# Optimization experiments

Hardware: AMD Instinct MI355X
Metric: run time of the kernel (lower is better)

Reference implementation:

```python
import jax, jax.numpy as jnp
import numpy as np

N = 4096
NFEAT = 512
NHID = 64
NHEADS = 8
NCLASS = 41
ALPHA = 0.2          # LeakyReLU negative slope
NEG = -9e15          # mask fill value from the torch code
EDGE_P = 0.004       # ~16 avg degree


def _xavier_uniform(key, shape, gain=1.414):
    fan_in, fan_out = shape[-2], shape[-1]
    limit = gain * np.sqrt(6.0 / (fan_in + fan_out))
    return jax.random.uniform(key, shape, jnp.float32, -limit, limit)


def setup_inputs() -> dict:
    key = jax.random.key(0)
    ks = jax.random.split(key, 6)
    x = jax.random.normal(ks[0], (N, NFEAT), jnp.float32)
    # sparse random graph, densified (module calls adj.to_dense()); add self-loops
    adj = (jax.random.uniform(ks[1], (N, N)) < EDGE_P).astype(jnp.float32)
    adj = jnp.maximum(adj, jnp.eye(N, dtype=jnp.float32))
    # 8 attention heads (nfeat -> nhid), stacked
    W_heads = _xavier_uniform(ks[2], (NHEADS, NFEAT, NHID))
    a_heads = _xavier_uniform(ks[3], (NHEADS, 2 * NHID, 1))
    # output attention layer (nhid*nheads -> nclass)
    W_out = _xavier_uniform(ks[4], (NHEADS * NHID, NCLASS))
    a_out = _xavier_uniform(ks[5], (2 * NCLASS, 1))
    return {"x": x, "adj": adj, "W_heads": W_heads, "a_heads": a_heads,
            "W_out": W_out, "a_out": a_out}


def _leaky_relu(e):
    return jnp.where(e > 0, e, ALPHA * e)


def reference(x, adj, W_heads, a_heads, W_out, a_out):
    # inference mode: all dropout layers are identity (training=False)
    mask = adj > 0                                   # [N, N]
    # ---- multi-head GAT layer (concat=True, ELU inside layer) ----
    Wh = jnp.einsum('nf,hfd->hnd', x, W_heads)       # [H, N, D]
    a1 = a_heads[:, :NHID, 0]                        # [H, D]
    a2 = a_heads[:, NHID:, 0]                        # [H, D]
    s1 = jnp.einsum('hnd,hd->hn', Wh, a1)            # [H, N]
    s2 = jnp.einsum('hnd,hd->hn', Wh, a2)            # [H, N]
    e = _leaky_relu(s1[:, :, None] + s2[:, None, :])  # [H, N, N]
    att = jax.nn.softmax(jnp.where(mask[None], e, NEG), axis=-1)
    h = jax.nn.elu(jnp.einsum('hnm,hmd->hnd', att, Wh))   # [H, N, D]
    h = jnp.transpose(h, (1, 0, 2)).reshape(N, NHEADS * NHID)  # concat heads
    # ---- output GAT layer (concat=False) + ELU (with_relu=True) ----
    Wh2 = h @ W_out                                  # [N, C]
    e2 = _leaky_relu(Wh2 @ a_out[:NCLASS] + (Wh2 @ a_out[NCLASS:]).T)  # [N, N]
    att2 = jax.nn.softmax(jnp.where(mask, e2, NEG), axis=-1)
    out = jax.nn.elu(att2 @ Wh2)                     # [N, C]
    # mode='t', multi_label falsy -> log_softmax
    return jax.nn.log_softmax(out, axis=1)
```

## Files before the change

kernel.cpp:

```cpp
#include <hip/hip_runtime.h>
#include <hip/hip_bf16.h>
#include <math.h>


#define N 4096
#define NFEAT 512
#define NHID 64
#define NHEADS 8
#define NCLASS 41
#define NCPAD 48
#define ALPHA 0.2f
#define ELLW 64

using short8  = __attribute__((ext_vector_type(8))) short;
using floatx4 = __attribute__((ext_vector_type(4))) float;

__device__ __forceinline__ float wred_max(float v) {
#pragma unroll
  for (int o = 32; o; o >>= 1) v = fmaxf(v, __shfl_xor(v, o, 64));
  return v;
}
__device__ __forceinline__ float wred_sum(float v) {
#pragma unroll
  for (int o = 32; o; o >>= 1) v += __shfl_xor(v, o, 64);
  return v;
}

__device__ __forceinline__ void split_bf16(float v, short& hi, short& lo) {
  __hip_bfloat16 hb = __float2bfloat16(v);
  float hf = __bfloat162float(hb);
  __hip_bfloat16 lb = __float2bfloat16(v - hf);
  hi = *reinterpret_cast<short*>(&hb);
  lo = *reinterpret_cast<short*>(&lb);
}

__global__ __launch_bounds__(256) void setup(const float* __restrict__ x,
                                             const float* __restrict__ W,
                                             const float* __restrict__ W_out,
                                             const float* __restrict__ adj,
                                             short* __restrict__ Xhi,
                                             short* __restrict__ Xlo,
                                             short* __restrict__ Wthi,
                                             short* __restrict__ Wtlo,
                                             short* __restrict__ WOhi,
                                             short* __restrict__ WOlo,
                                             int* __restrict__ cols,
                                             int* __restrict__ cnts) {
  if (blockIdx.x < 4096) {
    __shared__ int c;
    const int row = blockIdx.x;
    if (threadIdx.x == 0) c = 0;
    __syncthreads();
    const float4* arow = (const float4*)(adj + (size_t)row * N);
    for (int j4 = threadIdx.x; j4 < N / 4; j4 += 256) {
      float4 v = arow[j4];
      if (v.x > 0.f) { int p = atomicAdd(&c, 1); if (p < ELLW) cols[row * ELLW + p] = j4 * 4 + 0; }
      if (v.y > 0.f) { int p = atomicAdd(&c, 1); if (p < ELLW) cols[row * ELLW + p] = j4 * 4 + 1; }
      if (v.z > 0.f) { int p = atomicAdd(&c, 1); if (p < ELLW) cols[row * ELLW + p] = j4 * 4 + 2; }
      if (v.w > 0.f) { int p = atomicAdd(&c, 1); if (p < ELLW) cols[row * ELLW + p] = j4 * 4 + 3; }
    }
    __syncthreads();
    if (threadIdx.x == 0) cnts[row] = min(c, ELLW);
  } else if (blockIdx.x < 6144) {
    const int t = (blockIdx.x - 4096) * 256 + threadIdx.x;
    const float4 v = ((const float4*)x)[t];
    short h0, l0, h1, l1, h2, l2, h3, l3;
    split_bf16(v.x, h0, l0);
    split_bf16(v.y, h1, l1);
    split_bf16(v.z, h2, l2);
    split_bf16(v.w, h3, l3);
    ((short4*)Xhi)[t] = make_short4(h0, h1, h2, h3);
    ((short4*)Xlo)[t] = make_short4(l0, l1, l2, l3);
  } else if (blockIdx.x < 6208) {
    __shared__ float tile[64][65];
    const int idx = blockIdx.x - 6144;
    const int h = idx >> 3, k0 = (idx & 7) * 64;
    const int t = threadIdx.x;
#pragma unroll
    for (int i = 0; i < 4; i++) {
      const int g = t + 256 * i;
      const int r = g >> 4, c4 = g & 15;
      const float4 v = *(const float4*)&W[(size_t)h * 32768 + (size_t)(k0 + r) * 64 + c4 * 4];
      tile[r][c4 * 4 + 0] = v.x;
      tile[r][c4 * 4 + 1] = v.y;
      tile[r][c4 * 4 + 2] = v.z;
      tile[r][c4 * 4 + 3] = v.w;
    }
    __syncthreads();
#pragma unroll
    for (int i = 0; i < 2; i++) {
      const int g = t + 256 * i;
      const int d = g >> 3, kg = (g & 7) * 8;
      short8 hv, lv;
#pragma unroll
      for (int j = 0; j < 8; j++) {
        short hh, ll;
        split_bf16(tile[kg + j][d], hh, ll);
        hv[j] = hh;
        lv[j] = ll;
      }
      const size_t dst = (size_t)h * 32768 + (size_t)d * 512 + k0 + kg;
      *(short8*)&Wthi[dst] = hv;
      *(short8*)&Wtlo[dst] = lv;
    }
  } else {
    const int t = (blockIdx.x - 6208) * 256 + threadIdx.x;
    const int c = t >> 9, k = t & 511;
    float v = (c < NCLASS) ? W_out[(size_t)k * NCLASS + c] : 0.f;
    short hi, lo;
    split_bf16(v, hi, lo);
    WOhi[c * 512 + k] = hi;
    WOlo[c * 512 + k] = lo;
  }
}

__global__ __launch_bounds__(256) void wh_gemm_mfma(
    const short* __restrict__ Xhi, const short* __restrict__ Xlo,
    const short* __restrict__ Wthi, const short* __restrict__ Wtlo,
    const float* __restrict__ a_heads,
    float* __restrict__ Wh, float* __restrict__ s1, float* __restrict__ s2) {
  const int id = blockIdx.x;
  const int h = (id >> 3) & 7;
  const int tile = (id & 7) + ((id >> 6) << 3);
  const int n0 = tile * 64;
  const int w = threadIdx.x >> 6, L = threadIdx.x & 63;
  const int q = L >> 4, r15 = L & 15;

  floatx4 acc[4];
#pragma unroll
  for (int f = 0; f < 4; f++) acc[f] = (floatx4){0.f, 0.f, 0.f, 0.f};

  const short* Ah = Xhi + (size_t)(n0 + w * 16 + r15) * NFEAT;
  const short* Al = Xlo + (size_t)(n0 + w * 16 + r15) * NFEAT;
  const short* Bh = Wthi + (size_t)h * 32768 + (size_t)r15 * 512;
  const short* Bl = Wtlo + (size_t)h * 32768 + (size_t)r15 * 512;

#pragma unroll 2
  for (int ks = 0; ks < 16; ks++) {
    const int ko = ks * 32 + q * 8;
    const short8 ahi = *(const short8*)&Ah[ko];
    const short8 alo = *(const short8*)&Al[ko];
#pragma unroll
    for (int f = 0; f < 4; f++) {
      const short8 bhi = *(const short8*)&Bh[f * 16 * 512 + ko];
      const short8 blo = *(const short8*)&Bl[f * 16 * 512 + ko];
      acc[f] = __builtin_amdgcn_mfma_f32_16x16x32_bf16(ahi, bhi, acc[f], 0, 0, 0);
      acc[f] = __builtin_amdgcn_mfma_f32_16x16x32_bf16(ahi, blo, acc[f], 0, 0, 0);
      acc[f] = __builtin_amdgcn_mfma_f32_16x16x32_bf16(alo, bhi, acc[f], 0, 0, 0);
    }
  }

  const int c16 = r15;
  float a1v[4], a2v[4];
#pragma unroll
  for (int f = 0; f < 4; f++) {
    a1v[f] = a_heads[h * 128 + f * 16 + c16];
    a2v[f] = a_heads[h * 128 + 64 + f * 16 + c16];
  }
  float p1[4] = {0.f, 0.f, 0.f, 0.f}, p2[4] = {0.f, 0.f, 0.f, 0.f};
#pragma unroll
  for (int f = 0; f < 4; f++)
#pragma unroll
    for (int r = 0; r < 4; r++) {
      const float vv = acc[f][r];
      const int row = n0 + w * 16 + q * 4 + r;
      Wh[((size_t)(h << 12) + row) * NHID + f * 16 + c16] = vv;
      p1[r] += vv * a1v[f];
      p2[r] += vv * a2v[f];
    }
#pragma unroll
  for (int r = 0; r < 4; r++)
#pragma unroll
    for (int o = 1; o < 16; o <<= 1) {
      p1[r] += __shfl_xor(p1[r], o, 64);
      p2[r] += __shfl_xor(p2[r], o, 64);
    }
  if (c16 == 0) {
    const int row = n0 + w * 16 + q * 4;
#pragma unroll
    for (int r = 0; r < 4; r++) {
      s1[(h << 12) + row + r] = p1[r];
      s2[(h << 12) + row + r] = p2[r];
    }
  }
}

__global__ __launch_bounds__(256) void att1_kernel(
    const float* __restrict__ Wh, const float* __restrict__ s1,
    const float* __restrict__ s2, const int* __restrict__ cols,
    const int* __restrict__ cnts, short* __restrict__ Hhi,
    short* __restrict__ Hlo) {
  __shared__ float pj[4][64];
  __shared__ int jj[4][64];
  const int w = threadIdx.x >> 6, lane = threadIdx.x & 63;
  const int pair = blockIdx.x * 4 + w;
  const int h = pair >> 12, i = pair & (N - 1);
  const int cnt = cnts[i];
  const float s1i = s1[(h << 12) + i];
  const float* s2h = s2 + (h << 12);
  float e0 = -1e30f;
  int j0 = 0;
  if (lane < cnt) {
    j0 = cols[i * ELLW + lane];
    float t = s1i + s2h[j0];
    e0 = t > 0.f ? t : ALPHA * t;
  }
  const float m = wred_max(e0);
  float p = (lane < cnt) ? expf(e0 - m) : 0.f;
  const float S = wred_sum(p);
  p *= 1.f / S;
  pj[w][lane] = p;
  jj[w][lane] = (lane < cnt) ? j0 : 0;
  __syncthreads();
  const int grp = lane >> 3, c8 = lane & 7;
  const float* Whh = Wh + (((size_t)h << 12)) * NHID;
  float4 a0 = make_float4(0.f, 0.f, 0.f, 0.f);
  float4 a1 = make_float4(0.f, 0.f, 0.f, 0.f);
  for (int t0 = 0; t0 < cnt; t0 += 8) {
    const float pt = pj[w][t0 + grp];
    const int jt = jj[w][t0 + grp];
    const float4 v0 = *(const float4*)&Whh[(size_t)jt * NHID + c8 * 8];
    const float4 v1 = *(const float4*)&Whh[(size_t)jt * NHID + c8 * 8 + 4];
    a0.x += pt * v0.x; a0.y += pt * v0.y; a0.z += pt * v0.z; a0.w += pt * v0.w;
    a1.x += pt * v1.x; a1.y += pt * v1.y; a1.z += pt * v1.z; a1.w += pt * v1.w;
  }
#pragma unroll
  for (int off = 8; off <= 32; off <<= 1) {
    a0.x += __shfl_xor(a0.x, off, 64);
    a0.y += __shfl_xor(a0.y, off, 64);
    a0.z += __shfl_xor(a0.z, off, 64);
    a0.w += __shfl_xor(a0.w, off, 64);
    a1.x += __shfl_xor(a1.x, off, 64);
    a1.y += __shfl_xor(a1.y, off, 64);
    a1.z += __shfl_xor(a1.z, off, 64);
    a1.w += __shfl_xor(a1.w, off, 64);
  }
  if (grp == 0) {
    float o[8] = {a0.x, a0.y, a0.z, a0.w, a1.x, a1.y, a1.z, a1.w};
    short8 hv, lv;
#pragma unroll
    for (int j = 0; j < 8; j++) {
      const float e = o[j] > 0.f ? o[j] : expf(o[j]) - 1.f;
      short hh, ll;
      split_bf16(e, hh, ll);
      hv[j] = hh;
      lv[j] = ll;
    }
    const size_t base = (size_t)i * 512 + h * 64 + c8 * 8;
    *(short8*)&Hhi[base] = hv;
    *(short8*)&Hlo[base] = lv;
  }
}

__global__ __launch_bounds__(256) void gemm2_mfma(
    const short* __restrict__ Hhi, const short* __restrict__ Hlo,
    const short* __restrict__ WOhi, const short* __restrict__ WOlo,
    const float* __restrict__ a_out,
    float* __restrict__ Wh2, float* __restrict__ s1b, float* __restrict__ s2b) {
  __shared__ float red[3][64][12];
  const int n0 = blockIdx.x * 16;
  const int tid = threadIdx.x;
  const int w = tid >> 6, L = tid & 63;
  const int r15 = L & 15;

  floatx4 acc[3];
#pragma unroll
  for (int f = 0; f < 3; f++) acc[f] = (floatx4){0.f, 0.f, 0.f, 0.f};

#pragma unroll
  for (int ks = 0; ks < 4; ks++) {
    const int koff = w * 128 + ks * 32 + (L >> 4) * 8;
    const short8 ahi = *(const short8*)&Hhi[(size_t)(n0 + r15) * 512 + koff];
    const short8 alo = *(const short8*)&Hlo[(size_t)(n0 + r15) * 512 + koff];
#pragma unroll
    for (int f = 0; f < 3; f++) {
      const short8 bhi = *(const short8*)&WOhi[(size_t)(f * 16 + r15) * 512 + koff];
      const short8 blo = *(const short8*)&WOlo[(size_t)(f * 16 + r15) * 512 + koff];
      acc[f] = __builtin_amdgcn_mfma_f32_16x16x32_bf16(ahi, bhi, acc[f], 0, 0, 0);
      acc[f] = __builtin_amdgcn_mfma_f32_16x16x32_bf16(ahi, blo, acc[f], 0, 0, 0);
      acc[f] = __builtin_amdgcn_mfma_f32_16x16x32_bf16(alo, bhi, acc[f], 0, 0, 0);
    }
  }

  if (w) {
#pragma unroll
    for (int f = 0; f < 3; f++)
#pragma unroll
      for (int r = 0; r < 4; r++) red[w - 1][L][f * 4 + r] = acc[f][r];
  }
  __syncthreads();
  if (w == 0) {
    const int q = L >> 4, c16 = r15;
    float a1v[3], a2v[3];
#pragma unroll
    for (int f = 0; f < 3; f++) {
      const int col = f * 16 + c16;
      a1v[f] = (col < NCLASS) ? a_out[col] : 0.f;
      a2v[f] = (col < NCLASS) ? a_out[NCLASS + col] : 0.f;
    }
    float p1[4] = {0.f, 0.f, 0.f, 0.f}, p2[4] = {0.f, 0.f, 0.f, 0.f};
#pragma unroll
    for (int f = 0; f < 3; f++)
#pragma unroll
      for (int r = 0; r < 4; r++) {
        const float vv = acc[f][r] + red[0][L][f * 4 + r] + red[1][L][f * 4 + r] +
                         red[2][L][f * 4 + r];
        const int col = f * 16 + c16;
        const int row = n0 + q * 4 + r;
        if (col < NCLASS) Wh2[(size_t)row * NCLASS + col] = vv;
        p1[r] += vv * a1v[f];
        p2[r] += vv * a2v[f];
      }
#pragma unroll
    for (int r = 0; r < 4; r++)
#pragma unroll
      for (int o = 1; o < 16; o <<= 1) {
        p1[r] += __shfl_xor(p1[r], o, 64);
        p2[r] += __shfl_xor(p2[r], o, 64);
      }
    if (c16 == 0) {
      const int row = n0 + q * 4;
#pragma unroll
      for (int r = 0; r < 4; r++) {
        s1b[row + r] = p1[r];
        s2b[row + r] = p2[r];
      }
    }
  }
}

__global__ __launch_bounds__(256) void att2_kernel(const float* __restrict__ Wh2,
                                                   const float* __restrict__ s1b,
                                                   const float* __restrict__ s2b,
                                                   const int* __restrict__ cols,
                                                   const int* __restrict__ cnts,
                                                   float* __restrict__ out) {
  __shared__ float pj[4][64];
  __shared__ int jj[4][64];
  const int w = threadIdx.x >> 6, lane = threadIdx.x & 63;
  const int i = blockIdx.x * 4 + w;
  const int cnt = cnts[i];
  const float s1i = s1b[i];
  float e0 = -1e30f;
  int j0 = 0;
  if (lane < cnt) {
    j0 = cols[i * ELLW + lane];
    float t = s1i + s2b[j0];
    e0 = t > 0.f ? t : ALPHA * t;
  }
  const float m = wred_max(e0);
  float p = (lane < cnt) ? expf(e0 - m) : 0.f;
  const float S = wred_sum(p);
  p *= 1.f / S;
  pj[w][lane] = p;
  jj[w][lane] = (lane < cnt) ? j0 : 0;
  __syncthreads();
  float acc = 0.f;
  for (int t = 0; t < cnt; t++) {
    const float pt = pj[w][t];
    const int jt = jj[w][t];
    if (lane < NCLASS) acc += pt * Wh2[(size_t)jt * NCLASS + lane];
  }
  const float o = acc > 0.f ? acc : expf(acc) - 1.f;
  const float vv = (lane < NCLASS) ? o : -1e30f;
  const float mm = wred_max(vv);
  const float ex = (lane < NCLASS) ? expf(o - mm) : 0.f;
  const float SS = wred_sum(ex);
  if (lane < NCLASS) out[(size_t)i * NCLASS + lane] = o - mm - logf(SS);
}

extern "C" void kernel_launch(void* const* d_in, const int* in_sizes, int n_in,
                              void* d_out, int out_size, void* d_ws, size_t ws_size,
                              hipStream_t stream) {
  const float* x       = (const float*)d_in[0];
  const float* adj     = (const float*)d_in[1];
  const float* W_heads = (const float*)d_in[2];
  const float* a_heads = (const float*)d_in[3];
  const float* W_out   = (const float*)d_in[4];
  const float* a_out   = (const float*)d_in[5];
  float* out = (float*)d_out;

  float* ws   = (float*)d_ws;
  float* Wh   = ws;
  float* s1   = Wh + (size_t)NHEADS * N * NHID;
  float* s2   = s1 + NHEADS * N;
  float* Wh2  = s2 + NHEADS * N;
  float* s1b  = Wh2 + (size_t)N * NCLASS;
  float* s2b  = s1b + N;
  int* cnts   = (int*)(s2b + N);
  int* cols   = cnts + N;
  short* Xhi  = (short*)(cols + N * ELLW);
  short* Xlo  = Xhi + (size_t)N * NFEAT;
  short* Wthi = Xlo + (size_t)N * NFEAT;
  short* Wtlo = Wthi + (size_t)NHEADS * NHID * NFEAT;
  short* WOhi = Wtlo + (size_t)NHEADS * NHID * NFEAT;
  short* WOlo = WOhi + (size_t)NCPAD * 512;
  short* Hhi  = WOlo + (size_t)NCPAD * 512;
  short* Hlo  = Hhi + (size_t)N * NFEAT;

  hipLaunchKernelGGL(setup, dim3(6304), dim3(256), 0, stream,
                     x, W_heads, W_out, adj, Xhi, Xlo, Wthi, Wtlo, WOhi, WOlo, cols, cnts);
  hipLaunchKernelGGL(wh_gemm_mfma, dim3(NHEADS * N / 64), dim3(256), 0, stream,
                     Xhi, Xlo, Wthi, Wtlo, a_heads, Wh, s1, s2);
  hipLaunchKernelGGL(att1_kernel, dim3(NHEADS * N / 4), dim3(256), 0, stream,
                     Wh, s1, s2, cols, cnts, Hhi, Hlo);
  hipLaunchKernelGGL(gemm2_mfma, dim3(N / 16), dim3(256), 0, stream,
                     Hhi, Hlo, WOhi, WOlo, a_out, Wh2, s1b, s2b);
  hipLaunchKernelGGL(att2_kernel, dim3(N / 4), dim3(256), 0, stream,
                     Wh2, s1b, s2b, cols, cnts, out);
}
```

Before: 184.8 us.

## Split K across waves in Wh GEMM with shared-memory reduction

The Wh GEMM now gives each block 16 rows, and its four waves each handle a quarter of the K dimension. Partial accumulators go through shared memory and wave 0 sums them before computing the attention scores. Grid size grows fourfold (2048 blocks) to raise parallelism and shorten each wave's serial K loop. In exchange it adds an LDS reduction and a barrier, leaves three waves idle during the epilogue, and reloads each B tile in four times as many blocks.

```diff
diff --git a/kernel.cpp b/kernel.cpp
--- a/kernel.cpp
+++ b/kernel.cpp
@@ -114,15 +114,15 @@
   }
 }
 
-__global__ __launch_bounds__(256) void wh_gemm_mfma(
+__global__ __launch_bounds__(256, 4) void wh_gemm_mfma(
     const short* __restrict__ Xhi, const short* __restrict__ Xlo,
     const short* __restrict__ Wthi, const short* __restrict__ Wtlo,
     const float* __restrict__ a_heads,
     float* __restrict__ Wh, float* __restrict__ s1, float* __restrict__ s2) {
+  __shared__ float red[3][64][16];
   const int id = blockIdx.x;
-  const int h = (id >> 3) & 7;
-  const int tile = (id & 7) + ((id >> 6) << 3);
-  const int n0 = tile * 64;
+  const int h = id & 7;
+  const int n0 = (id >> 3) * 16;
   const int w = threadIdx.x >> 6, L = threadIdx.x & 63;
   const int q = L >> 4, r15 = L & 15;
 
@@ -130,14 +130,14 @@
 #pragma unroll
   for (int f = 0; f < 4; f++) acc[f] = (floatx4){0.f, 0.f, 0.f, 0.f};
 
-  const short* Ah = Xhi + (size_t)(n0 + w * 16 + r15) * NFEAT;
-  const short* Al = Xlo + (size_t)(n0 + w * 16 + r15) * NFEAT;
+  const short* Ah = Xhi + (size_t)(n0 + r15) * NFEAT;
+  const short* Al = Xlo + (size_t)(n0 + r15) * NFEAT;
   const short* Bh = Wthi + (size_t)h * 32768 + (size_t)r15 * 512;
   const short* Bl = Wtlo + (size_t)h * 32768 + (size_t)r15 * 512;
 
 #pragma unroll 2
-  for (int ks = 0; ks < 16; ks++) {
-    const int ko = ks * 32 + q * 8;
+  for (int ks = 0; ks < 4; ks++) {
+    const int ko = w * 128 + ks * 32 + q * 8;
     const short8 ahi = *(const short8*)&Ah[ko];
     const short8 alo = *(const short8*)&Al[ko];
 #pragma unroll
@@ -150,37 +150,47 @@
     }
   }
 
-  const int c16 = r15;
-  float a1v[4], a2v[4];
-#pragma unroll
-  for (int f = 0; f < 4; f++) {
-    a1v[f] = a_heads[h * 128 + f * 16 + c16];
-    a2v[f] = a_heads[h * 128 + 64 + f * 16 + c16];
-  }
-  float p1[4] = {0.f, 0.f, 0.f, 0.f}, p2[4] = {0.f, 0.f, 0.f, 0.f};
-#pragma unroll
-  for (int f = 0; f < 4; f++)
-#pragma unroll
-    for (int r = 0; r < 4; r++) {
-      const float vv = acc[f][r];
-      const int row = n0 + w * 16 + q * 4 + r;
-      Wh[((size_t)(h << 12) + row) * NHID + f * 16 + c16] = vv;
-      p1[r] += vv * a1v[f];
-      p2[r] += vv * a2v[f];
-    }
-#pragma unroll
-  for (int r = 0; r < 4; r++)
-#pragma unroll
-    for (int o = 1; o < 16; o <<= 1) {
-      p1[r] += __shfl_xor(p1[r], o, 64);
-      p2[r] += __shfl_xor(p2[r], o, 64);
-    }
-  if (c16 == 0) {
-    const int row = n0 + w * 16 + q * 4;
-#pragma unroll
-    for (int r = 0; r < 4; r++) {
-      s1[(h << 12) + row + r] = p1[r];
-      s2[(h << 12) + row + r] = p2[r];
+  if (w) {
+#pragma unroll
+    for (int f = 0; f < 4; f++)
+#pragma unroll
+      for (int r = 0; r < 4; r++) red[w - 1][L][f * 4 + r] = acc[f][r];
+  }
+  __syncthreads();
+  if (w == 0) {
+    const int c16 = r15;
+    float a1v[4], a2v[4];
+#pragma unroll
+    for (int f = 0; f < 4; f++) {
+      a1v[f] = a_heads[h * 128 + f * 16 + c16];
+      a2v[f] = a_heads[h * 128 + 64 + f * 16 + c16];
+    }
+    float p1[4] = {0.f, 0.f, 0.f, 0.f}, p2[4] = {0.f, 0.f, 0.f, 0.f};
+#pragma unroll
+    for (int f = 0; f < 4; f++)
+#pragma unroll
+      for (int r = 0; r < 4; r++) {
+        const float vv = acc[f][r] + red[0][L][f * 4 + r] + red[1][L][f * 4 + r] +
+                         red[2][L][f * 4 + r];
+        const int row = n0 + q * 4 + r;
+        Wh[((size_t)(h << 12) + row) * NHID + f * 16 + c16] = vv;
+        p1[r] += vv * a1v[f];
+        p2[r] += vv * a2v[f];
+      }
+#pragma unroll
+    for (int r = 0; r < 4; r++)
+#pragma unroll
+      for (int o = 1; o < 16; o <<= 1) {
+        p1[r] += __shfl_xor(p1[r], o, 64);
+        p2[r] += __shfl_xor(p2[r], o, 64);
+      }
+    if (c16 == 0) {
+      const int row = n0 + q * 4;
+#pragma unroll
+      for (int r = 0; r < 4; r++) {
+        s1[(h << 12) + row + r] = p1[r];
+        s2[(h << 12) + row + r] = p2[r];
+      }
     }
   }
 }
@@ -400,7 +410,7 @@
 
   hipLaunchKernelGGL(setup, dim3(6304), dim3(256), 0, stream,
                      x, W_heads, W_out, adj, Xhi, Xlo, Wthi, Wtlo, WOhi, WOlo, cols, cnts);
-  hipLaunchKernelGGL(wh_gemm_mfma, dim3(NHEADS * N / 64), dim3(256), 0, stream,
+  hipLaunchKernelGGL(wh_gemm_mfma, dim3(NHEADS * N / 16), dim3(256), 0, stream,
                      Xhi, Xlo, Wthi, Wtlo, a_heads, Wh, s1, s2);
   hipLaunchKernelGGL(att1_kernel, dim3(NHEADS * N / 4), dim3(256), 0, stream,
                      Wh, s1, s2, cols, cnts, Hhi, Hlo);
```

Result: no change. 183.5 us (-0.7%).
